# Kernel optimization log

Measured on AMD Instinct MI355X. Metric: run time of the kernel, lower is better.

## Reference

```python
import jax, jax.numpy as jnp
import numpy as np

L, B, D, H = 1024, 128, 256, 256


def setup_inputs() -> dict:
    key = jax.random.key(0)
    k1, k2, k3, k4, k5 = jax.random.split(key, 5)
    bound_x = 1.0 / np.sqrt(D)
    bound_h = 1.0 / np.sqrt(H)
    return {
        "x": jax.random.normal(k1, (L, B, D), dtype=jnp.float32),
        "h": jnp.zeros((B, H), dtype=jnp.float32),
        "Wx_w": jax.random.uniform(k2, (H, D), jnp.float32, -bound_x, bound_x),
        "Wx_b": jax.random.uniform(k3, (H,), jnp.float32, -bound_x, bound_x),
        "Wh_w": jax.random.uniform(k4, (H, H), jnp.float32, -bound_h, bound_h),
        "Wh_b": jax.random.uniform(k5, (H,), jnp.float32, -bound_h, bound_h),
    }


def reference(x, h, Wx_w, Wx_b, Wh_w, Wh_b):
    # Precompute input projections for all timesteps in one big GEMM:
    # [L,B,D] @ [D,H] -> [L,B,H]
    xproj = jnp.einsum('lbd,hd->lbh', x, Wx_w) + Wx_b

    def step(h_prev, xp_t):
        # Elman step: h_t = tanh(Wx x_t + b_x + Wh h_{t-1} + b_h)
        h_new = jnp.tanh(xp_t + h_prev @ Wh_w.T + Wh_b)
        return h_new, h_new

    h_final, hAll = jax.lax.scan(step, h, xproj)
    return hAll, h_final
```

## Files before the change

kernel.cpp:

```cpp
#include <hip/hip_runtime.h>
#include <cstddef>

#define L_SEQ 1024
#define B_SZ  128
#define D_SZ  256
#define H_SZ  256

#define KT  16
#define LDA 132

__global__ __launch_bounds__(256) void xproj_gemm(
    const float* __restrict__ x, const float* __restrict__ Wx,
    const float* __restrict__ bx, float* __restrict__ out)
{
    __shared__ float sA[KT][LDA];
    __shared__ float sB[KT][LDA];

    const int tm  = blockIdx.x;
    const int tn  = blockIdx.y;
    const int tid = threadIdx.x;
    const int tx  = tid & 15;
    const int ty  = tid >> 4;
    const int srow = tid >> 2;
    const int skq  = tid & 3;

    const float* __restrict__ Ag = x  + (size_t)(tm * 128 + srow) * D_SZ + skq * 4;
    const float* __restrict__ Bg = Wx + (size_t)(tn * 128 + srow) * D_SZ + skq * 4;

    float c[2][2][4][4];
    #pragma unroll
    for (int mc = 0; mc < 2; ++mc)
        #pragma unroll
        for (int nc = 0; nc < 2; ++nc)
            #pragma unroll
            for (int i = 0; i < 4; ++i)
                #pragma unroll
                for (int j = 0; j < 4; ++j) c[mc][nc][i][j] = 0.0f;

    for (int kt = 0; kt < D_SZ / KT; ++kt) {
        float4 av0 = *reinterpret_cast<const float4*>(Ag + kt * KT);
        float4 av1 = *reinterpret_cast<const float4*>(Ag + (size_t)64 * D_SZ + kt * KT);
        float4 bv0 = *reinterpret_cast<const float4*>(Bg + kt * KT);
        float4 bv1 = *reinterpret_cast<const float4*>(Bg + (size_t)64 * D_SZ + kt * KT);
        __syncthreads();
        sA[skq * 4 + 0][srow] = av0.x; sA[skq * 4 + 1][srow] = av0.y;
        sA[skq * 4 + 2][srow] = av0.z; sA[skq * 4 + 3][srow] = av0.w;
        sA[skq * 4 + 0][64 + srow] = av1.x; sA[skq * 4 + 1][64 + srow] = av1.y;
        sA[skq * 4 + 2][64 + srow] = av1.z; sA[skq * 4 + 3][64 + srow] = av1.w;
        sB[skq * 4 + 0][srow] = bv0.x; sB[skq * 4 + 1][srow] = bv0.y;
        sB[skq * 4 + 2][srow] = bv0.z; sB[skq * 4 + 3][srow] = bv0.w;
        sB[skq * 4 + 0][64 + srow] = bv1.x; sB[skq * 4 + 1][64 + srow] = bv1.y;
        sB[skq * 4 + 2][64 + srow] = bv1.z; sB[skq * 4 + 3][64 + srow] = bv1.w;
        __syncthreads();
        #pragma unroll
        for (int kk = 0; kk < KT; ++kk) {
            float4 am0 = *reinterpret_cast<const float4*>(&sA[kk][ty * 4]);
            float4 am1 = *reinterpret_cast<const float4*>(&sA[kk][64 + ty * 4]);
            float4 bn0 = *reinterpret_cast<const float4*>(&sB[kk][tx * 4]);
            float4 bn1 = *reinterpret_cast<const float4*>(&sB[kk][64 + tx * 4]);
            float aa[2][4] = {{am0.x, am0.y, am0.z, am0.w}, {am1.x, am1.y, am1.z, am1.w}};
            float bb[2][4] = {{bn0.x, bn0.y, bn0.z, bn0.w}, {bn1.x, bn1.y, bn1.z, bn1.w}};
            #pragma unroll
            for (int mc = 0; mc < 2; ++mc)
                #pragma unroll
                for (int nc = 0; nc < 2; ++nc)
                    #pragma unroll
                    for (int i = 0; i < 4; ++i)
                        #pragma unroll
                        for (int j = 0; j < 4; ++j)
                            c[mc][nc][i][j] = fmaf(aa[mc][i], bb[nc][j], c[mc][nc][i][j]);
        }
    }

    #pragma unroll
    for (int nc = 0; nc < 2; ++nc) {
        float4 bias = *reinterpret_cast<const float4*>(bx + tn * 128 + nc * 64 + tx * 4);
        #pragma unroll
        for (int mc = 0; mc < 2; ++mc)
            #pragma unroll
            for (int i = 0; i < 4; ++i) {
                float4 v;
                v.x = c[mc][nc][i][0] + bias.x;
                v.y = c[mc][nc][i][1] + bias.y;
                v.z = c[mc][nc][i][2] + bias.z;
                v.w = c[mc][nc][i][3] + bias.w;
                *reinterpret_cast<float4*>(
                    out + (size_t)(tm * 128 + mc * 64 + ty * 4 + i) * H_SZ
                        + tn * 128 + nc * 64 + tx * 4) = v;
            }
    }
}

#define SLICE_W 40

typedef float f2 __attribute__((ext_vector_type(2)));

#define PKFMA(acc, w, h) \
    asm("v_pk_fma_f32 %0, %1, %2, %0" : "+v"(acc) : "v"(w), "v"(h))

template <int CTRL>
__device__ __forceinline__ float dpp_add(float v) {
    int y = __builtin_amdgcn_mov_dpp(__float_as_int(v), CTRL, 0xf, 0xf, true);
    return v + __int_as_float(y);
}
__device__ __forceinline__ float red8(f2 a) {
    float v = a.x + a.y;
    v = dpp_add<0xB1>(v);
    v = dpp_add<0x4E>(v);
    v = dpp_add<0x141>(v);
    return v;
}
__device__ __forceinline__ float fast_tanh(float x) {
    float e = __expf(2.0f * x);
    return 1.0f - 2.0f * __builtin_amdgcn_rcpf(e + 1.0f);
}

__device__ __forceinline__ void lds_barrier() {
    asm volatile("s_waitcnt lgkmcnt(0)" ::: "memory");
    __builtin_amdgcn_s_barrier();
    asm volatile("" ::: "memory");
}

#define DECLQ(c, q) \
    f2 w##c##_##q##l = r##c[2 * (q)], w##c##_##q##h = r##c[2 * (q) + 1];
#define DECLC(c) \
    DECLQ(c,0) DECLQ(c,1) DECLQ(c,2) DECLQ(c,3) \
    DECLQ(c,4) DECLQ(c,5) DECLQ(c,6) DECLQ(c,7)

#define FMAQ(q) { \
    float4 hv = hv4[q]; \
    f2 hlo = {hv.x, hv.y}; \
    f2 hhi = {hv.z, hv.w}; \
    PKFMA(a0, w0_##q##l, hlo); PKFMA(a0, w0_##q##h, hhi); \
    PKFMA(a1, w1_##q##l, hlo); PKFMA(a1, w1_##q##h, hhi); \
    PKFMA(a2, w2_##q##l, hlo); PKFMA(a2, w2_##q##h, hhi); \
    PKFMA(a3, w3_##q##l, hlo); PKFMA(a3, w3_##q##h, hhi); }

#define BODY(T, SRC, DST, X0, X1, X2, X3) { \
    float u0 = X0 + bj0, u1 = X1 + bj1, u2 = X2 + bj2, u3 = X3 + bj3; \
    { \
        const int tnext = (T) + 2 < L_SEQ ? (T) + 2 : L_SEQ - 1; \
        const size_t t2 = (size_t)tnext * tstr; \
        X0 = outb[t2 + jg +   0]; \
        X1 = outb[t2 + jg +  64]; \
        X2 = outb[t2 + jg + 128]; \
        X3 = outb[t2 + jg + 192]; \
    } \
    f2 a0 = {0.f, 0.f}, a1 = {0.f, 0.f}, a2 = {0.f, 0.f}, a3 = {0.f, 0.f}; \
    const float4* hv4 = reinterpret_cast<const float4*>(&hs[SRC][ks * SLICE_W]); \
    FMAQ(0) FMAQ(1) FMAQ(2) FMAQ(3) FMAQ(4) FMAQ(5) FMAQ(6) FMAQ(7) \
    float s0 = red8(a0); \
    float s1 = red8(a1); \
    float s2 = red8(a2); \
    float s3 = red8(a3); \
    hn0 = fast_tanh(u0 + s0); \
    hn1 = fast_tanh(u1 + s1); \
    hn2 = fast_tanh(u2 + s2); \
    hn3 = fast_tanh(u3 + s3); \
    if (ks == 0) { \
        const size_t tb = (size_t)(T) * tstr; \
        __builtin_nontemporal_store(hn0, &outb[tb + jg +   0]); \
        __builtin_nontemporal_store(hn1, &outb[tb + jg +  64]); \
        __builtin_nontemporal_store(hn2, &outb[tb + jg + 128]); \
        __builtin_nontemporal_store(hn3, &outb[tb + jg + 192]); \
        float* hw = hs[DST]; \
        const int base = (jg >> 5) * SLICE_W + (jg & 31); \
        hw[base + 0 * (2 * SLICE_W)] = hn0; \
        hw[base + 1 * (2 * SLICE_W)] = hn1; \
        hw[base + 2 * (2 * SLICE_W)] = hn2; \
        hw[base + 3 * (2 * SLICE_W)] = hn3; \
    } \
    lds_barrier(); \
}

__global__ __launch_bounds__(512)
__attribute__((amdgpu_waves_per_eu(2, 2)))
void rnn_scan(
    const float* __restrict__ h0, const float* __restrict__ Wh,
    const float* __restrict__ bh, float* __restrict__ out)
{
    __shared__ __align__(16) float hs[2][8 * SLICE_W];

    const int b    = blockIdx.x;
    const int tid  = threadIdx.x;
    const int lane = tid & 63;
    const int wave = tid >> 6;
    const int ks   = lane & 7;
    const int jg   = wave * 8 + (lane >> 3);

    const f2* r0 = reinterpret_cast<const f2*>(Wh + (size_t)(jg +   0) * H_SZ + ks * 32);
    const f2* r1 = reinterpret_cast<const f2*>(Wh + (size_t)(jg +  64) * H_SZ + ks * 32);
    const f2* r2 = reinterpret_cast<const f2*>(Wh + (size_t)(jg + 128) * H_SZ + ks * 32);
    const f2* r3 = reinterpret_cast<const f2*>(Wh + (size_t)(jg + 192) * H_SZ + ks * 32);
    DECLC(0) DECLC(1) DECLC(2) DECLC(3)

    const float bj0 = bh[jg +   0];
    const float bj1 = bh[jg +  64];
    const float bj2 = bh[jg + 128];
    const float bj3 = bh[jg + 192];

    if (tid < H_SZ) {
        hs[0][(tid >> 5) * SLICE_W + (tid & 31)] = h0[(size_t)b * H_SZ + tid];
    }
    __syncthreads();

    float* __restrict__ outb = out + (size_t)b * H_SZ;
    const size_t tstr = (size_t)B_SZ * H_SZ;

    float xa0 = outb[jg +   0];
    float xa1 = outb[jg +  64];
    float xa2 = outb[jg + 128];
    float xa3 = outb[jg + 192];
    float xb0 = outb[tstr + jg +   0];
    float xb1 = outb[tstr + jg +  64];
    float xb2 = outb[tstr + jg + 128];
    float xb3 = outb[tstr + jg + 192];

    float hn0 = 0.f, hn1 = 0.f, hn2 = 0.f, hn3 = 0.f;
    for (int t = 0; t < L_SEQ; t += 2) {
        BODY(t,     0, 1, xa0, xa1, xa2, xa3)
        BODY(t + 1, 1, 0, xb0, xb1, xb2, xb3)
    }

    if (ks == 0) {
        float* hf = out + (size_t)L_SEQ * tstr + (size_t)b * H_SZ;
        hf[jg +   0] = hn0;
        hf[jg +  64] = hn1;
        hf[jg + 128] = hn2;
        hf[jg + 192] = hn3;
    }
}

extern "C" void kernel_launch(void* const* d_in, const int* in_sizes, int n_in,
                              void* d_out, int out_size, void* d_ws, size_t ws_size,
                              hipStream_t stream) {
    const float* x    = (const float*)d_in[0];
    const float* h0   = (const float*)d_in[1];
    const float* Wx_w = (const float*)d_in[2];
    const float* Wx_b = (const float*)d_in[3];
    const float* Wh_w = (const float*)d_in[4];
    const float* Wh_b = (const float*)d_in[5];
    float* out = (float*)d_out;

    (void)in_sizes; (void)n_in; (void)d_ws; (void)ws_size; (void)out_size;

    dim3 grid1((L_SEQ * B_SZ) / 128, H_SZ / 128);
    xproj_gemm<<<grid1, 256, 0, stream>>>(x, Wx_w, Wx_b, out);

    rnn_scan<<<dim3(B_SZ), 512, 0, stream>>>(h0, Wh_w, Wh_b, out);
}
```

Before: 1.025 ms.

## Fuse input-projection GEMM and recurrent scan into one producer-consumer kernel

Merges the two launches into one kernel. The first 128 blocks run the sequential scan; the remaining 2048 blocks compute one 128-row by 128-col tile of the input projection each. Each GEMM block signals completion per timestep through a flag counter in workspace, and the scan blocks spin on those flags before prefetching the next timestep's projection. This overlaps the GEMM with the recurrence instead of serialising them, and folds the hidden bias into the GEMM epilogue. In exchange it adds a memset, system-scope atomic polling and loads on the scan's critical path, and loses the waves-per-eu hint, so the shared register budget may cause spills. It also depends on the GEMM blocks getting scheduled alongside the resident scan blocks to avoid stalls.

```diff
diff --git a/kernel.cpp b/kernel.cpp
--- a/kernel.cpp
+++ b/kernel.cpp
@@ -6,91 +6,12 @@
 #define D_SZ  256
 #define H_SZ  256
 
+#define NSCAN 128
+#define NGEMM 2048
+
+
 #define KT  16
 #define LDA 132
-
-__global__ __launch_bounds__(256) void xproj_gemm(
-    const float* __restrict__ x, const float* __restrict__ Wx,
-    const float* __restrict__ bx, float* __restrict__ out)
-{
-    __shared__ float sA[KT][LDA];
-    __shared__ float sB[KT][LDA];
-
-    const int tm  = blockIdx.x;
-    const int tn  = blockIdx.y;
-    const int tid = threadIdx.x;
-    const int tx  = tid & 15;
-    const int ty  = tid >> 4;
-    const int srow = tid >> 2;
-    const int skq  = tid & 3;
-
-    const float* __restrict__ Ag = x  + (size_t)(tm * 128 + srow) * D_SZ + skq * 4;
-    const float* __restrict__ Bg = Wx + (size_t)(tn * 128 + srow) * D_SZ + skq * 4;
-
-    float c[2][2][4][4];
-    #pragma unroll
-    for (int mc = 0; mc < 2; ++mc)
-        #pragma unroll
-        for (int nc = 0; nc < 2; ++nc)
-            #pragma unroll
-            for (int i = 0; i < 4; ++i)
-                #pragma unroll
-                for (int j = 0; j < 4; ++j) c[mc][nc][i][j] = 0.0f;
-
-    for (int kt = 0; kt < D_SZ / KT; ++kt) {
-        float4 av0 = *reinterpret_cast<const float4*>(Ag + kt * KT);
-        float4 av1 = *reinterpret_cast<const float4*>(Ag + (size_t)64 * D_SZ + kt * KT);
-        float4 bv0 = *reinterpret_cast<const float4*>(Bg + kt * KT);
-        float4 bv1 = *reinterpret_cast<const float4*>(Bg + (size_t)64 * D_SZ + kt * KT);
-        __syncthreads();
-        sA[skq * 4 + 0][srow] = av0.x; sA[skq * 4 + 1][srow] = av0.y;
-        sA[skq * 4 + 2][srow] = av0.z; sA[skq * 4 + 3][srow] = av0.w;
-        sA[skq * 4 + 0][64 + srow] = av1.x; sA[skq * 4 + 1][64 + srow] = av1.y;
-        sA[skq * 4 + 2][64 + srow] = av1.z; sA[skq * 4 + 3][64 + srow] = av1.w;
-        sB[skq * 4 + 0][srow] = bv0.x; sB[skq * 4 + 1][srow] = bv0.y;
-        sB[skq * 4 + 2][srow] = bv0.z; sB[skq * 4 + 3][srow] = bv0.w;
-        sB[skq * 4 + 0][64 + srow] = bv1.x; sB[skq * 4 + 1][64 + srow] = bv1.y;
-        sB[skq * 4 + 2][64 + srow] = bv1.z; sB[skq * 4 + 3][64 + srow] = bv1.w;
-        __syncthreads();
-        #pragma unroll
-        for (int kk = 0; kk < KT; ++kk) {
-            float4 am0 = *reinterpret_cast<const float4*>(&sA[kk][ty * 4]);
-            float4 am1 = *reinterpret_cast<const float4*>(&sA[kk][64 + ty * 4]);
-            float4 bn0 = *reinterpret_cast<const float4*>(&sB[kk][tx * 4]);
-            float4 bn1 = *reinterpret_cast<const float4*>(&sB[kk][64 + tx * 4]);
-            float aa[2][4] = {{am0.x, am0.y, am0.z, am0.w}, {am1.x, am1.y, am1.z, am1.w}};
-            float bb[2][4] = {{bn0.x, bn0.y, bn0.z, bn0.w}, {bn1.x, bn1.y, bn1.z, bn1.w}};
-            #pragma unroll
-            for (int mc = 0; mc < 2; ++mc)
-                #pragma unroll
-                for (int nc = 0; nc < 2; ++nc)
-                    #pragma unroll
-                    for (int i = 0; i < 4; ++i)
-                        #pragma unroll
-                        for (int j = 0; j < 4; ++j)
-                            c[mc][nc][i][j] = fmaf(aa[mc][i], bb[nc][j], c[mc][nc][i][j]);
-        }
-    }
-
-    #pragma unroll
-    for (int nc = 0; nc < 2; ++nc) {
-        float4 bias = *reinterpret_cast<const float4*>(bx + tn * 128 + nc * 64 + tx * 4);
-        #pragma unroll
-        for (int mc = 0; mc < 2; ++mc)
-            #pragma unroll
-            for (int i = 0; i < 4; ++i) {
-                float4 v;
-                v.x = c[mc][nc][i][0] + bias.x;
-                v.y = c[mc][nc][i][1] + bias.y;
-                v.z = c[mc][nc][i][2] + bias.z;
-                v.w = c[mc][nc][i][3] + bias.w;
-                *reinterpret_cast<float4*>(
-                    out + (size_t)(tm * 128 + mc * 64 + ty * 4 + i) * H_SZ
-                        + tn * 128 + nc * 64 + tx * 4) = v;
-            }
-    }
-}
-
 #define SLICE_W 40
 
 typedef float f2 __attribute__((ext_vector_type(2)));
@@ -114,11 +35,94 @@
     float e = __expf(2.0f * x);
     return 1.0f - 2.0f * __builtin_amdgcn_rcpf(e + 1.0f);
 }
-
 __device__ __forceinline__ void lds_barrier() {
     asm volatile("s_waitcnt lgkmcnt(0)" ::: "memory");
     __builtin_amdgcn_s_barrier();
     asm volatile("" ::: "memory");
+}
+__device__ __forceinline__ float sysloadf(const float* p) {
+    return __hip_atomic_load(p, __ATOMIC_RELAXED, __HIP_MEMORY_SCOPE_SYSTEM);
+}
+__device__ __forceinline__ int sysloadi(const int* p) {
+    return __hip_atomic_load(p, __ATOMIC_RELAXED, __HIP_MEMORY_SCOPE_SYSTEM);
+}
+
+__device__ __forceinline__ void gemm_role(
+    int gb,
+    const float* __restrict__ x, const float* __restrict__ Wx,
+    const float* __restrict__ bx, const float* __restrict__ bh,
+    float* __restrict__ out, int* __restrict__ done,
+    float (*sA)[LDA], float (*sB)[LDA])
+{
+    const int tm  = gb >> 1;
+    const int tn  = gb & 1;
+    const int tid = threadIdx.x;
+    const int tx  = tid & 15;
+    const int ty  = tid >> 4;
+    const int srow = tid >> 2;
+    const int skq  = tid & 3;
+
+    const float* __restrict__ Ag = x  + (size_t)(tm * 128 + srow) * D_SZ + skq * 4;
+    const float* __restrict__ Bg = Wx + (size_t)(tn * 128 + srow) * D_SZ + skq * 4;
+
+    float c[2][4][4];
+    #pragma unroll
+    for (int nc = 0; nc < 2; ++nc)
+        #pragma unroll
+        for (int i = 0; i < 4; ++i)
+            #pragma unroll
+            for (int j = 0; j < 4; ++j) c[nc][i][j] = 0.0f;
+
+    for (int kt = 0; kt < D_SZ / KT; ++kt) {
+        float4 av = *reinterpret_cast<const float4*>(Ag + kt * KT);
+        float4 bv = *reinterpret_cast<const float4*>(Bg + kt * KT);
+        __syncthreads();
+        sA[skq * 4 + 0][srow] = av.x; sA[skq * 4 + 1][srow] = av.y;
+        sA[skq * 4 + 2][srow] = av.z; sA[skq * 4 + 3][srow] = av.w;
+        sB[skq * 4 + 0][srow] = bv.x; sB[skq * 4 + 1][srow] = bv.y;
+        sB[skq * 4 + 2][srow] = bv.z; sB[skq * 4 + 3][srow] = bv.w;
+        __syncthreads();
+        #pragma unroll
+        for (int kk = 0; kk < KT; ++kk) {
+            float4 am  = *reinterpret_cast<const float4*>(&sA[kk][ty * 4]);
+            float4 bn0 = *reinterpret_cast<const float4*>(&sB[kk][tx * 4]);
+            float4 bn1 = *reinterpret_cast<const float4*>(&sB[kk][64 + tx * 4]);
+            float aa[4] = {am.x, am.y, am.z, am.w};
+            float bb[2][4] = {{bn0.x, bn0.y, bn0.z, bn0.w},
+                              {bn1.x, bn1.y, bn1.z, bn1.w}};
+            #pragma unroll
+            for (int nc = 0; nc < 2; ++nc)
+                #pragma unroll
+                for (int i = 0; i < 4; ++i)
+                    #pragma unroll
+                    for (int j = 0; j < 4; ++j)
+                        c[nc][i][j] = fmaf(aa[i], bb[nc][j], c[nc][i][j]);
+        }
+    }
+
+    #pragma unroll
+    for (int nc = 0; nc < 2; ++nc) {
+        const int col = tn * 128 + nc * 64 + tx * 4;
+        float4 b4 = *reinterpret_cast<const float4*>(bx + col);
+        float4 h4 = *reinterpret_cast<const float4*>(bh + col);
+        #pragma unroll
+        for (int i = 0; i < 4; ++i) {
+            float4 v;
+            v.x = c[nc][i][0] + b4.x + h4.x;
+            v.y = c[nc][i][1] + b4.y + h4.y;
+            v.z = c[nc][i][2] + b4.z + h4.z;
+            v.w = c[nc][i][3] + b4.w + h4.w;
+            *reinterpret_cast<float4*>(
+                out + (size_t)(tm * 128 + ty * 4 + i) * H_SZ + col) = v;
+        }
+    }
+
+    __threadfence_system();
+    __syncthreads();
+    if (tid == 0) {
+        __hip_atomic_fetch_add(&done[tm], 1, __ATOMIC_RELEASE,
+                               __HIP_MEMORY_SCOPE_SYSTEM);
+    }
 }
 
 #define DECLQ(c, q) \
@@ -136,16 +140,24 @@
     PKFMA(a2, w2_##q##l, hlo); PKFMA(a2, w2_##q##h, hhi); \
     PKFMA(a3, w3_##q##l, hlo); PKFMA(a3, w3_##q##h, hhi); }
 
-#define BODY(T, SRC, DST, X0, X1, X2, X3) { \
-    float u0 = X0 + bj0, u1 = X1 + bj1, u2 = X2 + bj2, u3 = X3 + bj3; \
-    { \
-        const int tnext = (T) + 2 < L_SEQ ? (T) + 2 : L_SEQ - 1; \
-        const size_t t2 = (size_t)tnext * tstr; \
-        X0 = outb[t2 + jg +   0]; \
-        X1 = outb[t2 + jg +  64]; \
-        X2 = outb[t2 + jg + 128]; \
-        X3 = outb[t2 + jg + 192]; \
-    } \
+#define SBODY(T, SRC, DST, X0, X1, X2, X3) { \
+    if (la0 == 2) { ++hw; if (la1 == 2) ++hw; } \
+    const int tnext = ((T) + 2 < L_SEQ) ? (T) + 2 : L_SEQ - 1; \
+    { const int need = tnext + 1; \
+      while (hw < need) { \
+        int d = sysloadi(&done[hw]); \
+        if (d == 2) ++hw; else __builtin_amdgcn_s_sleep(2); \
+      } } \
+    asm volatile("" ::: "memory"); \
+    la0 = 0; la1 = 0; \
+    if (hw < L_SEQ)     la0 = sysloadi(&done[hw]); \
+    if (hw + 1 < L_SEQ) la1 = sysloadi(&done[hw + 1]); \
+    float u0 = X0, u1 = X1, u2 = X2, u3 = X3; \
+    { const size_t t2 = (size_t)tnext * tstr; \
+      X0 = sysloadf(&outb[t2 + jg +   0]); \
+      X1 = sysloadf(&outb[t2 + jg +  64]); \
+      X2 = sysloadf(&outb[t2 + jg + 128]); \
+      X3 = sysloadf(&outb[t2 + jg + 192]); } \
     f2 a0 = {0.f, 0.f}, a1 = {0.f, 0.f}, a2 = {0.f, 0.f}, a3 = {0.f, 0.f}; \
     const float4* hv4 = reinterpret_cast<const float4*>(&hs[SRC][ks * SLICE_W]); \
     FMAQ(0) FMAQ(1) FMAQ(2) FMAQ(3) FMAQ(4) FMAQ(5) FMAQ(6) FMAQ(7) \
@@ -163,25 +175,24 @@
         __builtin_nontemporal_store(hn1, &outb[tb + jg +  64]); \
         __builtin_nontemporal_store(hn2, &outb[tb + jg + 128]); \
         __builtin_nontemporal_store(hn3, &outb[tb + jg + 192]); \
-        float* hw = hs[DST]; \
+        float* hptr = hs[DST]; \
         const int base = (jg >> 5) * SLICE_W + (jg & 31); \
-        hw[base + 0 * (2 * SLICE_W)] = hn0; \
-        hw[base + 1 * (2 * SLICE_W)] = hn1; \
-        hw[base + 2 * (2 * SLICE_W)] = hn2; \
-        hw[base + 3 * (2 * SLICE_W)] = hn3; \
+        hptr[base + 0 * (2 * SLICE_W)] = hn0; \
+        hptr[base + 1 * (2 * SLICE_W)] = hn1; \
+        hptr[base + 2 * (2 * SLICE_W)] = hn2; \
+        hptr[base + 3 * (2 * SLICE_W)] = hn3; \
     } \
     lds_barrier(); \
 }
 
-__global__ __launch_bounds__(512)
-__attribute__((amdgpu_waves_per_eu(2, 2)))
-void rnn_scan(
+__device__ __forceinline__ void scan_role(
+    int b,
     const float* __restrict__ h0, const float* __restrict__ Wh,
-    const float* __restrict__ bh, float* __restrict__ out)
+    float* __restrict__ out, int* __restrict__ done,
+    float (*hs)[8 * SLICE_W])
 {
-    __shared__ __align__(16) float hs[2][8 * SLICE_W];
-
-    const int b    = blockIdx.x;
+    __builtin_amdgcn_s_setprio(1);
+
     const int tid  = threadIdx.x;
     const int lane = tid & 63;
     const int wave = tid >> 6;
@@ -194,11 +205,6 @@
     const f2* r3 = reinterpret_cast<const f2*>(Wh + (size_t)(jg + 192) * H_SZ + ks * 32);
     DECLC(0) DECLC(1) DECLC(2) DECLC(3)
 
-    const float bj0 = bh[jg +   0];
-    const float bj1 = bh[jg +  64];
-    const float bj2 = bh[jg + 128];
-    const float bj3 = bh[jg + 192];
-
     if (tid < H_SZ) {
         hs[0][(tid >> 5) * SLICE_W + (tid & 31)] = h0[(size_t)b * H_SZ + tid];
     }
@@ -207,19 +213,26 @@
     float* __restrict__ outb = out + (size_t)b * H_SZ;
     const size_t tstr = (size_t)B_SZ * H_SZ;
 
-    float xa0 = outb[jg +   0];
-    float xa1 = outb[jg +  64];
-    float xa2 = outb[jg + 128];
-    float xa3 = outb[jg + 192];
-    float xb0 = outb[tstr + jg +   0];
-    float xb1 = outb[tstr + jg +  64];
-    float xb2 = outb[tstr + jg + 128];
-    float xb3 = outb[tstr + jg + 192];
+    int hw = 0, la0 = 0, la1 = 0;
+    while (hw < 2) {
+        int d = sysloadi(&done[hw]);
+        if (d == 2) ++hw; else __builtin_amdgcn_s_sleep(8);
+    }
+    asm volatile("" ::: "memory");
+
+    float xa0 = sysloadf(&outb[jg +   0]);
+    float xa1 = sysloadf(&outb[jg +  64]);
+    float xa2 = sysloadf(&outb[jg + 128]);
+    float xa3 = sysloadf(&outb[jg + 192]);
+    float xb0 = sysloadf(&outb[tstr + jg +   0]);
+    float xb1 = sysloadf(&outb[tstr + jg +  64]);
+    float xb2 = sysloadf(&outb[tstr + jg + 128]);
+    float xb3 = sysloadf(&outb[tstr + jg + 192]);
 
     float hn0 = 0.f, hn1 = 0.f, hn2 = 0.f, hn3 = 0.f;
     for (int t = 0; t < L_SEQ; t += 2) {
-        BODY(t,     0, 1, xa0, xa1, xa2, xa3)
-        BODY(t + 1, 1, 0, xb0, xb1, xb2, xb3)
+        SBODY(t,     0, 1, xa0, xa1, xa2, xa3)
+        SBODY(t + 1, 1, 0, xb0, xb1, xb2, xb3)
     }
 
     if (ks == 0) {
@@ -228,6 +241,24 @@
         hf[jg +  64] = hn1;
         hf[jg + 128] = hn2;
         hf[jg + 192] = hn3;
+    }
+}
+
+__global__ __launch_bounds__(512) void rnn_fused(
+    const float* __restrict__ x,  const float* __restrict__ h0,
+    const float* __restrict__ Wx, const float* __restrict__ bx,
+    const float* __restrict__ Wh, const float* __restrict__ bh,
+    float* __restrict__ out, int* __restrict__ done)
+{
+    __shared__ float sA[KT][LDA];
+    __shared__ float sB[KT][LDA];
+    __shared__ __align__(16) float hs[2][8 * SLICE_W];
+
+    const int bid = blockIdx.x;
+    if (bid < NSCAN) {
+        scan_role(bid, h0, Wh, out, done, hs);
+    } else {
+        gemm_role(bid - NSCAN, x, Wx, bx, bh, out, done, sA, sB);
     }
 }
 
@@ -241,11 +272,12 @@
     const float* Wh_w = (const float*)d_in[4];
     const float* Wh_b = (const float*)d_in[5];
     float* out = (float*)d_out;
-
-    (void)in_sizes; (void)n_in; (void)d_ws; (void)ws_size; (void)out_size;
-
-    dim3 grid1((L_SEQ * B_SZ) / 128, H_SZ / 128);
-    xproj_gemm<<<grid1, 256, 0, stream>>>(x, Wx_w, Wx_b, out);
-
-    rnn_scan<<<dim3(B_SZ), 512, 0, stream>>>(h0, Wh_w, Wh_b, out);
-}
+    int* done = (int*)d_ws;
+
+    (void)in_sizes; (void)n_in; (void)ws_size; (void)out_size;
+
+    hipMemsetAsync(done, 0, L_SEQ * sizeof(int), stream);
+
+    rnn_fused<<<dim3(NSCAN + NGEMM), 512, 0, stream>>>(
+        x, h0, Wx_w, Wx_b, Wh_w, Wh_b, out, done);
+}
```

Result: slower. 1.549 ms (+51.2%).
